# Kernel tuning notes

Hardware: AMD Instinct MI355X
Metric: run time of the kernel (lower is better)

Reference implementation:

```python
import jax, jax.numpy as jnp
import numpy as np
import math

B, N, H, NH, HD, G = 2, 1024, 512, 8, 64, 50
MAX_DIST = 10.0


def setup_inputs() -> dict:
    key = jax.random.key(0)
    ks = jax.random.split(key, 12)
    s = 0.02  # small init scale for weights
    return {
        'x': jax.random.normal(ks[0], (B, N, H), jnp.float32),
        'distances': jax.random.uniform(ks[1], (B, N, N), jnp.float32) * MAX_DIST,
        'mask': jnp.ones((B, N), jnp.int32),
        'widths': jnp.ones((G,), jnp.float32) * 0.5,
        'dp_w': jax.random.normal(ks[2], (G, NH), jnp.float32) * s,
        'dp_b': jnp.zeros((NH,), jnp.float32),
        'wq': jax.random.normal(ks[3], (H, H), jnp.float32) * s,
        'bq': jnp.zeros((H,), jnp.float32),
        'wk': jax.random.normal(ks[4], (H, H), jnp.float32) * s,
        'bk': jnp.zeros((H,), jnp.float32),
        'wv': jax.random.normal(ks[5], (H, H), jnp.float32) * s,
        'bv': jnp.zeros((H,), jnp.float32),
        'wo': jax.random.normal(ks[6], (H, H), jnp.float32) * s,
        'bo': jnp.zeros((H,), jnp.float32),
        'ln1_g': jnp.ones((H,), jnp.float32),
        'ln1_b': jnp.zeros((H,), jnp.float32),
        'ln2_g': jnp.ones((H,), jnp.float32),
        'ln2_b': jnp.zeros((H,), jnp.float32),
        'w1': jax.random.normal(ks[7], (H, 4 * H), jnp.float32) * s,
        'b1': jnp.zeros((4 * H,), jnp.float32),
        'w2': jax.random.normal(ks[8], (4 * H, H), jnp.float32) * s,
        'b2': jnp.zeros((H,), jnp.float32),
    }


def _layernorm(x, g, b, eps=1e-5):
    mu = jnp.mean(x, axis=-1, keepdims=True)
    var = jnp.mean(jnp.square(x - mu), axis=-1, keepdims=True)
    return (x - mu) * jax.lax.rsqrt(var + eps) * g + b


def reference(x, distances, mask, widths, dp_w, dp_b, wq, bq, wk, bk, wv, bv,
              wo, bo, ln1_g, ln1_b, ln2_g, ln2_b, w1, b1, w2, b2):
    centers = jnp.linspace(0.0, MAX_DIST, G, dtype=jnp.float32)  # buffer

    residual = x
    xn = _layernorm(x, ln1_g, ln1_b)

    def split_heads(t):  # [B,N,H] -> [B,NH,N,HD]
        return t.reshape(B, N, NH, HD).transpose(0, 2, 1, 3)

    q = split_heads(xn @ wq + bq)
    k = split_heads(xn @ wk + bk)
    v = split_heads(xn @ wv + bv)

    scores = jnp.einsum('bhqd,bhkd->bhqk', q, k) / math.sqrt(HD)

    # Gaussian distance encoding: [B,N,N,G]
    diff = distances[..., None] - centers
    gf = jnp.exp(-jnp.square(diff) / (2.0 * jnp.square(widths)))
    # project to per-head bias, then permute to [B,NH,N,N]
    dist_bias = (gf @ dp_w + dp_b).transpose(0, 3, 1, 2)
    scores = scores + dist_bias

    key_mask = mask[:, None, None, :]  # [B,1,1,N]
    scores = jnp.where(key_mask == 0, -1e9, scores)

    attn = jax.nn.softmax(scores, axis=-1)
    out = jnp.einsum('bhqk,bhkd->bhqd', attn, v)
    out = out.transpose(0, 2, 1, 3).reshape(B, N, H)
    out = out @ wo + bo

    x = residual + out
    residual = x
    xn = _layernorm(x, ln2_g, ln2_b)
    h = jax.nn.gelu(xn @ w1 + b1, approximate=False)  # dropout is identity in eval
    x = residual + (h @ w2 + b2)
    return x
```

## Files before the change

### kernel.cpp

```cpp
#include <hip/hip_runtime.h>
#include <hip/hip_bf16.h>
#include <math.h>

#define B_ 2
#define N_ 1024
#define H_ 512
#define NH_ 8
#define HD_ 64
#define G_ 50
#define TAB_ 1024
constexpr float MAXD = 10.0f;

typedef __attribute__((ext_vector_type(8))) short short8;
typedef __attribute__((ext_vector_type(4))) float f32x4;

__device__ inline ushort f2bf(float v) {
  __hip_bfloat16 h = __float2bfloat16(v);
  return *(ushort*)&h;
}
__device__ inline float bf2f(ushort u) {
  unsigned x = ((unsigned)u) << 16;
  return __uint_as_float(x);
}
__device__ inline void gload_lds16(const ushort* g, ushort* l) {
  __builtin_amdgcn_global_load_lds(
      (const __attribute__((address_space(1))) void*)g,
      (__attribute__((address_space(3))) void*)l, 16, 0, 0);
}

__device__ inline void transp_dev(const float* __restrict__ src,
                                  ushort* __restrict__ d, int R, int C,
                                  int bx, int by, int t, float (*tile)[33]) {
  int r0 = by * 32, c0 = bx * 32;
  int rr = t >> 5, cc = t & 31;
  #pragma unroll
  for (int p = 0; p < 4; ++p)
    tile[rr + p * 8][cc] = src[(size_t)(r0 + rr + p * 8) * C + c0 + cc];
  __syncthreads();
  #pragma unroll
  for (int p = 0; p < 4; ++p)
    d[(size_t)(c0 + rr + p * 8) * R + r0 + cc] = f2bf(tile[cc][rr + p * 8]);
}

__global__ __launch_bounds__(256) void prep_k(
    const float* wq, const float* wk, const float* wv, const float* wo,
    const float* w1, const float* w2, ushort* __restrict__ wT4,
    ushort* __restrict__ w1T, ushort* __restrict__ w2T,
    const float* __restrict__ widths, const float* __restrict__ dp_w,
    const float* __restrict__ dp_b, float2* __restrict__ tab2,
    const float* __restrict__ x, const float* __restrict__ ln1g,
    const float* __restrict__ ln1b, ushort* __restrict__ xn) {
  __shared__ float tile[32][33];
  __shared__ float red2[4][2];
  int bid = blockIdx.x, t = threadIdx.x;
  if (bid < 1024) {
    int z = bid >> 8, rem = bid & 255;
    const float* src = (z == 0) ? wq : (z == 1) ? wk : (z == 2) ? wv : wo;
    transp_dev(src, wT4 + (size_t)z * 512 * 512, 512, 512, rem & 15, rem >> 4, t, tile);
  } else if (bid < 2048) {
    int rem = bid - 1024;
    transp_dev(w1, w1T, 512, 2048, rem & 63, rem >> 6, t, tile);
  } else if (bid < 3072) {
    int rem = bid - 2048;
    transp_dev(w2, w2T, 2048, 512, rem & 15, rem >> 4, t, tile);
  } else if (bid < 3105) {
    int i = (bid - 3072) * 256 + t;
    if (i >= NH_ * (TAB_ + 1)) return;
    int h = i / (TAB_ + 1), tt = i % (TAB_ + 1);
    int t1 = tt < TAB_ ? tt + 1 : tt;
    float d0 = (float)tt * (MAXD / TAB_);
    float d1 = (float)t1 * (MAXD / TAB_);
    float v0 = dp_b[h], v1 = dp_b[h];
    for (int g = 0; g < G_; ++g) {
      float c = (float)g * (MAXD / 49.0f);
      float w = widths[g];
      float inv = -1.0f / (2.0f * w * w);
      float wg = dp_w[g * NH_ + h];
      float e0 = d0 - c, e1 = d1 - c;
      v0 += expf(e0 * e0 * inv) * wg;
      v1 += expf(e1 * e1 * inv) * wg;
    }
    tab2[i] = make_float2(v0, v1);
  } else {
    int row = (bid - 3105) * 2 + (t >> 7);
    int tl = t & 127;
    float4 v = *(const float4*)(x + (size_t)row * H_ + tl * 4);
    float s = v.x + v.y + v.z + v.w;
    float sq = v.x * v.x + v.y * v.y + v.z * v.z + v.w * v.w;
    #pragma unroll
    for (int m = 1; m < 64; m <<= 1) {
      s += __shfl_xor(s, m, 64);
      sq += __shfl_xor(sq, m, 64);
    }
    int wid = t >> 6;
    if ((t & 63) == 0) { red2[wid][0] = s; red2[wid][1] = sq; }
    __syncthreads();
    int rw = (t >> 7) * 2;
    s = red2[rw][0] + red2[rw + 1][0];
    sq = red2[rw][1] + red2[rw + 1][1];
    float mu = s * (1.0f / H_);
    float var = sq * (1.0f / H_) - mu * mu;
    float rs = rsqrtf(var + 1e-5f);
    float4 gg = *(const float4*)(ln1g + tl * 4);
    float4 bb = *(const float4*)(ln1b + tl * 4);
    ushort4 o;
    o.x = f2bf((v.x - mu) * rs * gg.x + bb.x);
    o.y = f2bf((v.y - mu) * rs * gg.y + bb.y);
    o.z = f2bf((v.z - mu) * rs * gg.z + bb.z);
    o.w = f2bf((v.w - mu) * rs * gg.w + bb.w);
    *(ushort4*)(xn + (size_t)row * H_ + tl * 4) = o;
  }
}

enum { EPI_QKV = 1, EPI_RES = 2, EPI_GELU = 3, EPI_PART = 4 };

template <int BM, int BN, int EPI>
__global__ __launch_bounds__(256) void mfma_gemm(const ushort* __restrict__ A,
                                                 const ushort* __restrict__ Bt,
                                                 const float* __restrict__ b0,
                                                 const float* __restrict__ b1,
                                                 const float* __restrict__ b2,
                                                 const float* __restrict__ resid,
                                                 void* __restrict__ outv,
                                                 int K, int Ks, int Nc) {
  __shared__ ushort As[2][BM * 32];
  __shared__ ushort Bs[2][BN * 32];
  int t = threadIdx.x;
  int z = blockIdx.z;
  const ushort* Bz = Bt + (size_t)z * Nc * Ks;
  const float* bias = (z == 0) ? b0 : (z == 1) ? b1 : b2;
  int m0 = blockIdx.y * BM, n0 = blockIdx.x * BN;
  int lane = t & 63, w = t >> 6, wr = w >> 1, wc = w & 1;
  int lrow = lane & 15, lkg = lane >> 4;
  constexpr int NFM = BM / 32, NFN = BN / 32;
  constexpr int AL = BM / 64, BL = BN / 64;
  f32x4 acc[NFM][NFN] = {};
  int rl = lane >> 2, kgl = lane & 3;

  auto stage = [&](int buf, int kt) {
    #pragma unroll
    for (int p = 0; p < AL; ++p) {
      int r = w * (BM / 4) + p * 16 + rl;
      int kgs = kgl ^ (r & 3);
      gload_lds16(&A[(size_t)(m0 + r) * Ks + kt + kgs * 8],
                  &As[buf][(w * (BM / 4) + p * 16) * 32]);
    }
    #pragma unroll
    for (int p = 0; p < BL; ++p) {
      int r = w * (BN / 4) + p * 16 + rl;
      int kgs = kgl ^ (r & 3);
      gload_lds16(&Bz[(size_t)(n0 + r) * Ks + kt + kgs * 8],
                  &Bs[buf][(w * (BN / 4) + p * 16) * 32]);
    }
  };
  auto compute = [&](int buf) {
    short8 af[NFM], bfr[NFN];
    #pragma unroll
    for (int fm = 0; fm < NFM; ++fm) {
      int r = wr * (BM / 2) + fm * 16 + lrow;
      af[fm] = *(const short8*)&As[buf][r * 32 + ((lkg ^ (r & 3)) << 3)];
    }
    #pragma unroll
    for (int fn = 0; fn < NFN; ++fn) {
      int r = wc * (BN / 2) + fn * 16 + lrow;
      bfr[fn] = *(const short8*)&Bs[buf][r * 32 + ((lkg ^ (r & 3)) << 3)];
    }
    #pragma unroll
    for (int fm = 0; fm < NFM; ++fm)
      #pragma unroll
      for (int fn = 0; fn < NFN; ++fn)
        acc[fm][fn] = __builtin_amdgcn_mfma_f32_16x16x32_bf16(af[fm], bfr[fn],
                                                              acc[fm][fn], 0, 0, 0);
  };

  stage(0, 0);
  __syncthreads();
  int cur = 0;
  for (int kt = 0; kt < K; kt += 32) {
    if (kt + 32 < K) stage(cur ^ 1, kt + 32);
    compute(cur);
    __syncthreads();
    cur ^= 1;
  }

  int rbase = (lane >> 4) * 4;
  #pragma unroll
  for (int fm = 0; fm < NFM; ++fm) {
    #pragma unroll
    for (int fn = 0; fn < NFN; ++fn) {
      #pragma unroll
      for (int j = 0; j < 4; ++j) {
        int row = m0 + wr * (BM / 2) + fm * 16 + rbase + j;
        int col = n0 + wc * (BN / 2) + fn * 16 + lrow;
        float v = acc[fm][fn][j] + bias[col];
        if constexpr (EPI == EPI_QKV) {
          ushort* q = (ushort*)outv + (size_t)z * (1 << 20);
          int bb = row >> 10, n = row & (N_ - 1);
          int h = col >> 6, d = col & 63;
          if (z < 2)
            q[(((size_t)(bb * NH_ + h)) * N_ + n) * HD_ + d] = f2bf(v);
          else
            q[(((size_t)(bb * NH_ + h)) * HD_ + d) * N_ + n] = f2bf(v);
        } else if constexpr (EPI == EPI_RES) {
          ((float*)outv)[(size_t)row * Nc + col] =
              resid[(size_t)row * Nc + col] + v;
        } else {
          ((ushort*)outv)[(size_t)row * Nc + col] =
              f2bf(0.5f * v * (1.0f + erff(v * 0.70710678118654752f)));
        }
      }
    }
  }
}

template <int EPI>
__global__ __launch_bounds__(512) void mfma_gemm2(const ushort* __restrict__ A,
                                                  const ushort* __restrict__ Bt,
                                                  const float* __restrict__ bias,
                                                  const float* __restrict__ resid,
                                                  void* __restrict__ outv,
                                                  int K, int Ks, int Nc) {
  constexpr int BM = 64, BN = 64;
  __shared__ ushort AsBs[2][2][2][BM * 32];
  int t = threadIdx.x;
  int half = t >> 8;
  int lane = t & 63;
  int wl = (t >> 6) & 3;
  int wr = wl >> 1, wc = wl & 1;
  int lrow = lane & 15, lkg = lane >> 4;
  int k0 = half * K;
  int m0 = blockIdx.y * BM, n0 = blockIdx.x * BN;
  f32x4 acc[2][2] = {};
  int rl = lane >> 2, kgl = lane & 3;

  auto stage = [&](int buf, int kt) {
    int r = wl * 16 + rl;
    int kgs = kgl ^ (r & 3);
    gload_lds16(&A[(size_t)(m0 + r) * Ks + k0 + kt + kgs * 8],
                &AsBs[0][half][buf][(wl * 16) * 32]);
    gload_lds16(&Bt[(size_t)(n0 + r) * Ks + k0 + kt + kgs * 8],
                &AsBs[1][half][buf][(wl * 16) * 32]);
  };
  auto compute = [&](int buf) {
    short8 af[2], bfr[2];
    #pragma unroll
    for (int fm = 0; fm < 2; ++fm) {
      int r = wr * 32 + fm * 16 + lrow;
      af[fm] = *(const short8*)&AsBs[0][half][buf][r * 32 + ((lkg ^ (r & 3)) << 3)];
    }
    #pragma unroll
    for (int fn = 0; fn < 2; ++fn) {
      int r = wc * 32 + fn * 16 + lrow;
      bfr[fn] = *(const short8*)&AsBs[1][half][buf][r * 32 + ((lkg ^ (r & 3)) << 3)];
    }
    #pragma unroll
    for (int fm = 0; fm < 2; ++fm)
      #pragma unroll
      for (int fn = 0; fn < 2; ++fn)
        acc[fm][fn] = __builtin_amdgcn_mfma_f32_16x16x32_bf16(af[fm], bfr[fn],
                                                              acc[fm][fn], 0, 0, 0);
  };

  stage(0, 0);
  __syncthreads();
  int cur = 0;
  for (int kt = 0; kt < K; kt += 32) {
    if (kt + 32 < K) stage(cur ^ 1, kt + 32);
    compute(cur);
    __syncthreads();
    cur ^= 1;
  }

  float* red = (float*)&AsBs[0][0][0][0];
  int rbase = (lane >> 4) * 4;
  if (half == 1) {
    #pragma unroll
    for (int fm = 0; fm < 2; ++fm)
      #pragma unroll
      for (int fn = 0; fn < 2; ++fn)
        #pragma unroll
        for (int j = 0; j < 4; ++j) {
          int rloc = wr * 32 + fm * 16 + rbase + j;
          int cloc = wc * 32 + fn * 16 + lrow;
          red[rloc * 65 + cloc] = acc[fm][fn][j];
        }
  }
  __syncthreads();
  if (half == 0) {
    #pragma unroll
    for (int fm = 0; fm < 2; ++fm)
      #pragma unroll
      for (int fn = 0; fn < 2; ++fn)
        #pragma unroll
        for (int j = 0; j < 4; ++j) {
          int rloc = wr * 32 + fm * 16 + rbase + j;
          int cloc = wc * 32 + fn * 16 + lrow;
          float sum = acc[fm][fn][j] + red[rloc * 65 + cloc];
          int row = m0 + rloc, col = n0 + cloc;
          if constexpr (EPI == EPI_PART) {
            ((float*)outv)[(size_t)row * Nc + col] = sum;
          } else {
            ((float*)outv)[(size_t)row * Nc + col] =
                resid[(size_t)row * Nc + col] + sum + bias[col];
          }
        }
  }
}

__global__ __launch_bounds__(128) void comb2ln_k(const float* __restrict__ p,
                                                 const float* __restrict__ resid,
                                                 const float* __restrict__ bias,
                                                 const float* __restrict__ g,
                                                 const float* __restrict__ bl,
                                                 float* __restrict__ x1out,
                                                 ushort* __restrict__ xnout) {
  int row = blockIdx.x, t = threadIdx.x;
  int base = row * H_ + t * 4;
  f32x4 a = *(const f32x4*)&p[base];
  f32x4 r = *(const f32x4*)&resid[base];
  f32x4 bi = *(const f32x4*)&bias[t * 4];
  f32x4 v = r + a + bi;
  *(f32x4*)&x1out[base] = v;
  float s = v[0] + v[1] + v[2] + v[3];
  float sq = v[0] * v[0] + v[1] * v[1] + v[2] * v[2] + v[3] * v[3];
  #pragma unroll
  for (int m = 1; m < 64; m <<= 1) {
    s += __shfl_xor(s, m, 64);
    sq += __shfl_xor(sq, m, 64);
  }
  __shared__ float red[2][2];
  int wid = t >> 6;
  if ((t & 63) == 0) { red[wid][0] = s; red[wid][1] = sq; }
  __syncthreads();
  s = red[0][0] + red[1][0];
  sq = red[0][1] + red[1][1];
  float mu = s * (1.0f / H_);
  float var = sq * (1.0f / H_) - mu * mu;
  float rs = rsqrtf(var + 1e-5f);
  float4 gg = *(const float4*)(g + t * 4);
  float4 bb = *(const float4*)(bl + t * 4);
  ushort4 o;
  o.x = f2bf((v[0] - mu) * rs * gg.x + bb.x);
  o.y = f2bf((v[1] - mu) * rs * gg.y + bb.y);
  o.z = f2bf((v[2] - mu) * rs * gg.z + bb.z);
  o.w = f2bf((v[3] - mu) * rs * gg.w + bb.w);
  *(ushort4*)(xnout + (size_t)row * H_ + t * 4) = o;
}

constexpr int QT = 64, KT = 64, NJH = 2, NTH = N_ / (KT * NJH);
constexpr int JH = N_ / NJH;

__global__ __launch_bounds__(256) void attn_k(
    const ushort* __restrict__ q, const ushort* __restrict__ k,
    const ushort* __restrict__ v, const float* __restrict__ dist,
    const int* __restrict__ mask, const float2* __restrict__ tab2g,
    float* __restrict__ Op, float2* __restrict__ ml) {
  int qt = blockIdx.x, h = blockIdx.y, z = blockIdx.z;
  int b = z >> 1, jh = z & 1;
  int i0 = qt * QT;
  int jbase = jh * JH;
  __shared__ ushort Ks[2][KT * 64];
  __shared__ ushort Vt[2][64 * KT];
  __shared__ ushort Bsb[2][QT * 68];
  __shared__ ushort Ps[4][16 * 64];
  __shared__ float2 tl2[TAB_ + 1];
  __shared__ float mfl[JH];
  int t = threadIdx.x;
  int lane = t & 63, w = t >> 6;
  int l = lane & 15, g = lane >> 4;

  for (int i = t; i <= TAB_; i += 256) tl2[i] = tab2g[h * (TAB_ + 1) + i];
  for (int i = t; i < JH; i += 256) mfl[i] = (mask[b * N_ + jbase + i] == 0) ? -1e9f : 0.0f;

  const size_t ho = ((size_t)(b * NH_ + h)) * N_ * HD_;
  const ushort* qb = q + ho;
  const ushort* kb = k + ho;
  const ushort* vb = v + ho;

  int qrow = i0 + w * 16 + l;
  short8 qf[2];
  qf[0] = *(const short8*)&qb[(size_t)qrow * 64 + g * 8];
  qf[1] = *(const short8*)&qb[(size_t)qrow * 64 + 32 + g * 8];

  int c2 = t & 7, jr = t >> 3;
  int dr_r = t >> 2, dr_c = (t & 3) * 16;

  auto stK = [&](int buf, short8 val, int j2) {
    *(short8*)&Ks[buf][j2 * 64 + ((c2 ^ (j2 & 7)) << 3)] = val;
  };
  auto stV = [&](int buf, short8 val, int d) {
    *(short8*)&Vt[buf][d * 64 + ((c2 ^ (d & 7)) << 3)] = val;
  };

  short8 k0a, k1a, v0a, v1a;
  f32x4 dda[4];
  {
    const ushort* kn = kb + (size_t)jbase * 64;
    const ushort* vn = vb + jbase;
    k0a = *(const short8*)&kn[(size_t)jr * 64 + c2 * 8];
    k1a = *(const short8*)&kn[(size_t)(jr + 32) * 64 + c2 * 8];
    v0a = *(const short8*)&vn[(size_t)jr * N_ + c2 * 8];
    v1a = *(const short8*)&vn[(size_t)(jr + 32) * N_ + c2 * 8];
    const float* db = dist + ((size_t)b * N_ + (i0 + dr_r)) * N_ + jbase + dr_c;
    #pragma unroll
    for (int p = 0; p < 4; ++p) dda[p] = *(const f32x4*)&db[p * 4];
  }
  __syncthreads();
  {
    stK(0, k0a, jr); stK(0, k1a, jr + 32);
    stV(0, v0a, jr); stV(0, v1a, jr + 32);
    #pragma unroll
    for (int p = 0; p < 4; ++p) {
      ushort4 ov;
      #pragma unroll
      for (int e = 0; e < 4; ++e) {
        int jcol = dr_c + p * 4 + e;
        float u = dda[p][e] * ((float)TAB_ / MAXD);
        int it = (int)u;
        it = it < 0 ? 0 : (it > TAB_ - 1 ? TAB_ - 1 : it);
        float f = u - (float)it;
        float2 tv = tl2[it];
        ((ushort*)&ov)[e] = f2bf(tv.x + f * (tv.y - tv.x) + mfl[jcol]);
      }
      *(ushort4*)&Bsb[0][dr_r * 68 + dr_c + p * 4] = ov;
    }
  }
  __syncthreads();

  float m_[4] = {-1e30f, -1e30f, -1e30f, -1e30f};
  float l_[4] = {0.f, 0.f, 0.f, 0.f};
  f32x4 acc[4] = {{0,0,0,0},{0,0,0,0},{0,0,0,0},{0,0,0,0}};

  int cur = 0;
  for (int tt = 0; tt < NTH; ++tt) {
    const int j0 = jbase + tt * KT;
    if (tt + 1 < NTH) {
      const ushort* kn = kb + (size_t)(j0 + KT) * 64;
      const ushort* vn = vb + (j0 + KT);
      k0a = *(const short8*)&kn[(size_t)jr * 64 + c2 * 8];
      k1a = *(const short8*)&kn[(size_t)(jr + 32) * 64 + c2 * 8];
      v0a = *(const short8*)&vn[(size_t)jr * N_ + c2 * 8];
      v1a = *(const short8*)&vn[(size_t)(jr + 32) * N_ + c2 * 8];
      const float* db = dist + ((size_t)b * N_ + (i0 + dr_r)) * N_ + j0 + KT + dr_c;
      #pragma unroll
      for (int p = 0; p < 4; ++p) dda[p] = *(const f32x4*)&db[p * 4];
    }
    f32x4 sa[4] = {{0,0,0,0},{0,0,0,0},{0,0,0,0},{0,0,0,0}};
    __builtin_amdgcn_s_setprio(1);
    #pragma unroll
    for (int dblk = 0; dblk < 2; ++dblk)
      #pragma unroll
      for (int fj = 0; fj < 4; ++fj) {
        int j2 = fj * 16 + l;
        short8 kf = *(const short8*)&Ks[cur][j2 * 64 + (((dblk * 4 + g) ^ (j2 & 7)) << 3)];
        sa[fj] = __builtin_amdgcn_mfma_f32_16x16x32_bf16(qf[dblk], kf, sa[fj], 0, 0, 0);
      }
    __builtin_amdgcn_s_setprio(0);
    float al_[4];
    int qloc = w * 16 + 4 * g;
    #pragma unroll
    for (int reg = 0; reg < 4; ++reg) {
      float svr[4];
      #pragma unroll
      for (int fj = 0; fj < 4; ++fj)
        svr[fj] = fmaf(sa[fj][reg], 0.125f,
                       bf2f(Bsb[cur][(qloc + reg) * 68 + fj * 16 + l]));
      float rm = fmaxf(fmaxf(svr[0], svr[1]), fmaxf(svr[2], svr[3]));
      rm = fmaxf(rm, __shfl_xor(rm, 1, 64));
      rm = fmaxf(rm, __shfl_xor(rm, 2, 64));
      rm = fmaxf(rm, __shfl_xor(rm, 4, 64));
      rm = fmaxf(rm, __shfl_xor(rm, 8, 64));
      float mn = fmaxf(m_[reg], rm);
      float al = __expf(m_[reg] - mn);
      m_[reg] = mn;
      al_[reg] = al;
      float ps = 0.f;
      int qlq = 4 * g + reg;
      #pragma unroll
      for (int fj = 0; fj < 4; ++fj) {
        float p = __expf(svr[fj] - mn);
        ps += p;
        int c = fj * 2 + (l >> 3);
        Ps[w][qlq * 64 + ((c ^ (qlq & 7)) << 3) + (l & 7)] = f2bf(p);
      }
      ps += __shfl_xor(ps, 1, 64);
      ps += __shfl_xor(ps, 2, 64);
      ps += __shfl_xor(ps, 4, 64);
      ps += __shfl_xor(ps, 8, 64);
      l_[reg] = l_[reg] * al + ps;
    }
    #pragma unroll
    for (int fd = 0; fd < 4; ++fd)
      #pragma unroll
      for (int reg = 0; reg < 4; ++reg) acc[fd][reg] *= al_[reg];
    __builtin_amdgcn_s_setprio(1);
    #pragma unroll
    for (int jj = 0; jj < 2; ++jj) {
      short8 pa = *(const short8*)&Ps[w][l * 64 + (((jj * 4 + g) ^ (l & 7)) << 3)];
      #pragma unroll
      for (int fd = 0; fd < 4; ++fd) {
        int d2 = fd * 16 + l;
        short8 vf = *(const short8*)&Vt[cur][d2 * 64 + (((jj * 4 + g) ^ (d2 & 7)) << 3)];
        acc[fd] = __builtin_amdgcn_mfma_f32_16x16x32_bf16(pa, vf, acc[fd], 0, 0, 0);
      }
    }
    __builtin_amdgcn_s_setprio(0);
    if (tt + 1 < NTH) {
      int nb = cur ^ 1;
      stK(nb, k0a, jr); stK(nb, k1a, jr + 32);
      stV(nb, v0a, jr); stV(nb, v1a, jr + 32);
      const int jloc = (tt + 1) * KT;
      #pragma unroll
      for (int p = 0; p < 4; ++p) {
        ushort4 ov;
        #pragma unroll
        for (int e = 0; e < 4; ++e) {
          int jcol = dr_c + p * 4 + e;
          float u = dda[p][e] * ((float)TAB_ / MAXD);
          int it = (int)u;
          it = it < 0 ? 0 : (it > TAB_ - 1 ? TAB_ - 1 : it);
          float f = u - (float)it;
          float2 tv = tl2[it];
          ((ushort*)&ov)[e] = f2bf(tv.x + f * (tv.y - tv.x) + mfl[jloc + jcol]);
        }
        *(ushort4*)&Bsb[nb][dr_r * 68 + dr_c + p * 4] = ov;
      }
    }
    __syncthreads();
    cur ^= 1;
  }
  const size_t pbase = (((size_t)(b * NJH + jh) * NH_ + h) * N_) + i0;
  #pragma unroll
  for (int reg = 0; reg < 4; ++reg) {
    int rowl = w * 16 + 4 * g + reg;
    float* op = Op + (pbase + rowl) * HD_ + l;
    #pragma unroll
    for (int fd = 0; fd < 4; ++fd) op[fd * 16] = acc[fd][reg];
    if (l == 0) ml[pbase + rowl] = make_float2(m_[reg], l_[reg]);
  }
}

__global__ __launch_bounds__(256) void comb_k(const float* __restrict__ Op,
                                              const float2* __restrict__ ml,
                                              ushort* __restrict__ ao) {
  int idx = blockIdx.x * 256 + threadIdx.x;
  int row = idx >> 4;
  int dq = (idx & 15) * 4;
  int b = row >> 13, h = (row >> 10) & 7, n = row & 1023;
  size_t p0 = (((size_t)(b * NJH + 0) * NH_ + h) * N_) + n;
  size_t p1 = (((size_t)(b * NJH + 1) * NH_ + h) * N_) + n;
  float2 v0 = ml[p0], v1 = ml[p1];
  float M = fmaxf(v0.x, v1.x);
  float a0 = __expf(v0.x - M), a1 = __expf(v1.x - M);
  float inv = 1.0f / (v0.y * a0 + v1.y * a1);
  float4 O0 = *(const float4*)&Op[p0 * HD_ + dq];
  float4 O1 = *(const float4*)&Op[p1 * HD_ + dq];
  ushort4 o;
  o.x = f2bf((O0.x * a0 + O1.x * a1) * inv);
  o.y = f2bf((O0.y * a0 + O1.y * a1) * inv);
  o.z = f2bf((O0.z * a0 + O1.z * a1) * inv);
  o.w = f2bf((O0.w * a0 + O1.w * a1) * inv);
  *(ushort4*)&ao[((size_t)(b * N_ + n)) * H_ + h * HD_ + dq] = o;
}

extern "C" void kernel_launch(void* const* d_in, const int* in_sizes, int n_in,
                              void* d_out, int out_size, void* d_ws, size_t ws_size,
                              hipStream_t stream) {
  const float* x = (const float*)d_in[0];
  const float* distances = (const float*)d_in[1];
  const int* mask = (const int*)d_in[2];
  const float* widths = (const float*)d_in[3];
  const float* dp_w = (const float*)d_in[4];
  const float* dp_b = (const float*)d_in[5];
  const float* wq = (const float*)d_in[6];
  const float* bq = (const float*)d_in[7];
  const float* wk = (const float*)d_in[8];
  const float* bk = (const float*)d_in[9];
  const float* wv = (const float*)d_in[10];
  const float* bv = (const float*)d_in[11];
  const float* wo = (const float*)d_in[12];
  const float* bo = (const float*)d_in[13];
  const float* ln1_g = (const float*)d_in[14];
  const float* ln1_b = (const float*)d_in[15];
  const float* ln2_g = (const float*)d_in[16];
  const float* ln2_b = (const float*)d_in[17];
  const float* w1 = (const float*)d_in[18];
  const float* b1 = (const float*)d_in[19];
  const float* w2 = (const float*)d_in[20];
  const float* b2 = (const float*)d_in[21];
  float* out = (float*)d_out;
  float* wsf = (float*)d_ws;

  const size_t M1 = (size_t)1 << 20;
  ushort* qkvb = (ushort*)wsf;
  float* x1 = wsf + 2 * M1;
  ushort* hbuf = (ushort*)(wsf + 3 * M1);
  ushort* xn = (ushort*)(wsf + 5 * M1);
  ushort* xn2 = (ushort*)(wsf + 5 * M1 + M1 / 2);
  ushort* ao = (ushort*)(wsf + 6 * M1);
  ushort* wT4 = (ushort*)(wsf + 6 * M1 + M1 / 2);
  ushort* w1T = (ushort*)(wsf + 7 * M1);
  ushort* w2T = (ushort*)(wsf + 7 * M1 + M1 / 2);
  float2* tab2 = (float2*)(wsf + 8 * M1);
  float* Op = wsf + 9 * M1;
  float2* ml = (float2*)(wsf + 11 * M1);
  float* pAO = wsf + 12 * M1;

  prep_k<<<4129, 256, 0, stream>>>(wq, wk, wv, wo, w1, w2, wT4, w1T, w2T,
                                   widths, dp_w, dp_b, tab2, x, ln1_g, ln1_b, xn);

  mfma_gemm<64, 64, EPI_QKV><<<dim3(8, 32, 3), 256, 0, stream>>>(
      xn, wT4, bq, bk, bv, nullptr, qkvb, 512, 512, 512);

  attn_k<<<dim3(N_ / QT, NH_, B_ * NJH), 256, 0, stream>>>(
      qkvb, qkvb + M1, qkvb + 2 * M1, distances, mask, tab2, Op, ml);
  comb_k<<<1024, 256, 0, stream>>>(Op, ml, ao);

  mfma_gemm2<EPI_PART><<<dim3(8, 32), 512, 0, stream>>>(
      ao, wT4 + (size_t)3 * 512 * 512, bo, nullptr, pAO, 256, 512, 512);
  comb2ln_k<<<B_ * N_, 128, 0, stream>>>(pAO, x, bo, ln2_g, ln2_b, x1, xn2);

  mfma_gemm<128, 64, EPI_GELU><<<dim3(32, 16, 1), 256, 0, stream>>>(
      xn2, w1T, b1, b1, b1, nullptr, hbuf, 512, 512, 2048);

  mfma_gemm2<EPI_RES><<<dim3(8, 32), 512, 0, stream>>>(
      hbuf, w2T, b2, x1, out, 1024, 2048, 512);
}
```

Measured before the change: 98.81 us.

## Fuse split-KV attention combine into output projection GEMM A-load

Removes the separate combine kernel and the intermediate bf16 attention-output buffer by having the output-projection GEMM read the fp32 partial outputs and max/sum pairs directly. Each thread rescales the two partials, converts to bf16 and writes the swizzled LDS tile, prefetching the next tile's registers while computing the current one. This saves a launch and a round trip through memory, but the fp32 partials are reread by every column block, and exp/divide work is added inside the GEMM loop.

```diff
diff --git a/kernel.cpp b/kernel.cpp
--- a/kernel.cpp
+++ b/kernel.cpp
@@ -213,9 +213,11 @@
   }
 }
 
-template <int EPI>
+template <int EPI, bool CA>
 __global__ __launch_bounds__(512) void mfma_gemm2(const ushort* __restrict__ A,
                                                   const ushort* __restrict__ Bt,
+                                                  const float* __restrict__ Opp,
+                                                  const float2* __restrict__ mlp,
                                                   const float* __restrict__ bias,
                                                   const float* __restrict__ resid,
                                                   void* __restrict__ outv,
@@ -232,13 +234,44 @@
   int m0 = blockIdx.y * BM, n0 = blockIdx.x * BN;
   f32x4 acc[2][2] = {};
   int rl = lane >> 2, kgl = lane & 3;
-
-  auto stage = [&](int buf, int kt) {
-    int r = wl * 16 + rl;
-    int kgs = kgl ^ (r & 3);
-    gload_lds16(&A[(size_t)(m0 + r) * Ks + k0 + kt + kgs * 8],
+  int r_st = wl * 16 + rl;
+  int kgs_st = kgl ^ (r_st & 3);
+
+  f32x4 cO0a, cO0b, cO1a, cO1b;
+  float2 cml0, cml1;
+
+  auto loadA = [&](int kt) {
+    int row = m0 + r_st;
+    int bb = row >> 10, n = row & (N_ - 1);
+    int kb = k0 + kt + kgs_st * 8;
+    int h = kb >> 6, d = kb & 63;
+    size_t p0 = ((size_t)(bb * 2 + 0) * NH_ + h) * N_ + n;
+    size_t p1 = ((size_t)(bb * 2 + 1) * NH_ + h) * N_ + n;
+    cO0a = *(const f32x4*)&Opp[p0 * HD_ + d];
+    cO0b = *(const f32x4*)&Opp[p0 * HD_ + d + 4];
+    cO1a = *(const f32x4*)&Opp[p1 * HD_ + d];
+    cO1b = *(const f32x4*)&Opp[p1 * HD_ + d + 4];
+    cml0 = mlp[p0];
+    cml1 = mlp[p1];
+  };
+  auto writeA = [&](int buf) {
+    float M = fmaxf(cml0.x, cml1.x);
+    float a0 = __expf(cml0.x - M), a1 = __expf(cml1.x - M);
+    float inv = 1.0f / (cml0.y * a0 + cml1.y * a1);
+    short8 sv;
+    #pragma unroll
+    for (int i = 0; i < 4; ++i) {
+      sv[i] = (short)f2bf((cO0a[i] * a0 + cO1a[i] * a1) * inv);
+      sv[i + 4] = (short)f2bf((cO0b[i] * a0 + cO1b[i] * a1) * inv);
+    }
+    *(short8*)&AsBs[0][half][buf][r_st * 32 + kgl * 8] = sv;
+  };
+  auto stageA = [&](int buf, int kt) {
+    gload_lds16(&A[(size_t)(m0 + r_st) * Ks + k0 + kt + kgs_st * 8],
                 &AsBs[0][half][buf][(wl * 16) * 32]);
-    gload_lds16(&Bt[(size_t)(n0 + r) * Ks + k0 + kt + kgs * 8],
+  };
+  auto stageB = [&](int buf, int kt) {
+    gload_lds16(&Bt[(size_t)(n0 + r_st) * Ks + k0 + kt + kgs_st * 8],
                 &AsBs[1][half][buf][(wl * 16) * 32]);
   };
   auto compute = [&](int buf) {
@@ -261,12 +294,26 @@
                                                               acc[fm][fn], 0, 0, 0);
   };
 
-  stage(0, 0);
+  if constexpr (CA) {
+    loadA(0);
+    stageB(0, 0);
+    writeA(0);
+  } else {
+    stageA(0, 0);
+    stageB(0, 0);
+  }
   __syncthreads();
   int cur = 0;
   for (int kt = 0; kt < K; kt += 32) {
-    if (kt + 32 < K) stage(cur ^ 1, kt + 32);
-    compute(cur);
+    bool more = (kt + 32 < K);
+    if constexpr (CA) {
+      if (more) { loadA(kt + 32); stageB(cur ^ 1, kt + 32); }
+      compute(cur);
+      if (more) writeA(cur ^ 1);
+    } else {
+      if (more) { stageA(cur ^ 1, kt + 32); stageB(cur ^ 1, kt + 32); }
+      compute(cur);
+    }
     __syncthreads();
     cur ^= 1;
   }
@@ -538,29 +585,6 @@
     for (int fd = 0; fd < 4; ++fd) op[fd * 16] = acc[fd][reg];
     if (l == 0) ml[pbase + rowl] = make_float2(m_[reg], l_[reg]);
   }
-}
-
-__global__ __launch_bounds__(256) void comb_k(const float* __restrict__ Op,
-                                              const float2* __restrict__ ml,
-                                              ushort* __restrict__ ao) {
-  int idx = blockIdx.x * 256 + threadIdx.x;
-  int row = idx >> 4;
-  int dq = (idx & 15) * 4;
-  int b = row >> 13, h = (row >> 10) & 7, n = row & 1023;
-  size_t p0 = (((size_t)(b * NJH + 0) * NH_ + h) * N_) + n;
-  size_t p1 = (((size_t)(b * NJH + 1) * NH_ + h) * N_) + n;
-  float2 v0 = ml[p0], v1 = ml[p1];
-  float M = fmaxf(v0.x, v1.x);
-  float a0 = __expf(v0.x - M), a1 = __expf(v1.x - M);
-  float inv = 1.0f / (v0.y * a0 + v1.y * a1);
-  float4 O0 = *(const float4*)&Op[p0 * HD_ + dq];
-  float4 O1 = *(const float4*)&Op[p1 * HD_ + dq];
-  ushort4 o;
-  o.x = f2bf((O0.x * a0 + O1.x * a1) * inv);
-  o.y = f2bf((O0.y * a0 + O1.y * a1) * inv);
-  o.z = f2bf((O0.z * a0 + O1.z * a1) * inv);
-  o.w = f2bf((O0.w * a0 + O1.w * a1) * inv);
-  *(ushort4*)&ao[((size_t)(b * N_ + n)) * H_ + h * HD_ + dq] = o;
 }
 
 extern "C" void kernel_launch(void* const* d_in, const int* in_sizes, int n_in,
@@ -597,7 +621,6 @@
   ushort* hbuf = (ushort*)(wsf + 3 * M1);
   ushort* xn = (ushort*)(wsf + 5 * M1);
   ushort* xn2 = (ushort*)(wsf + 5 * M1 + M1 / 2);
-  ushort* ao = (ushort*)(wsf + 6 * M1);
   ushort* wT4 = (ushort*)(wsf + 6 * M1 + M1 / 2);
   ushort* w1T = (ushort*)(wsf + 7 * M1);
   ushort* w2T = (ushort*)(wsf + 7 * M1 + M1 / 2);
@@ -614,15 +637,14 @@
 
   attn_k<<<dim3(N_ / QT, NH_, B_ * NJH), 256, 0, stream>>>(
       qkvb, qkvb + M1, qkvb + 2 * M1, distances, mask, tab2, Op, ml);
-  comb_k<<<1024, 256, 0, stream>>>(Op, ml, ao);
-
-  mfma_gemm2<EPI_PART><<<dim3(8, 32), 512, 0, stream>>>(
-      ao, wT4 + (size_t)3 * 512 * 512, bo, nullptr, pAO, 256, 512, 512);
+
+  mfma_gemm2<EPI_PART, true><<<dim3(8, 32), 512, 0, stream>>>(
+      nullptr, wT4 + (size_t)3 * 512 * 512, Op, ml, bo, nullptr, pAO, 256, 512, 512);
   comb2ln_k<<<B_ * N_, 128, 0, stream>>>(pAO, x, bo, ln2_g, ln2_b, x1, xn2);
 
   mfma_gemm<128, 64, EPI_GELU><<<dim3(32, 16, 1), 256, 0, stream>>>(
       xn2, w1T, b1, b1, b1, nullptr, hbuf, 512, 512, 2048);
 
-  mfma_gemm2<EPI_RES><<<dim3(8, 32), 512, 0, stream>>>(
-      hbuf, w2T, b2, x1, out, 1024, 2048, 512);
-}
+  mfma_gemm2<EPI_RES, false><<<dim3(8, 32), 512, 0, stream>>>(
+      hbuf, w2T, nullptr, nullptr, b2, x1, out, 1024, 2048, 512);
+}
```

Measured after the change: 103.8 us. 1.05x slower.
